# Optimization experiments

Measured on AMD Instinct MI355X. Metric: run time of the kernel, lower is better.

Reference implementation:

```python
import jax, jax.numpy as jnp
import numpy as np

B, S, E, H, W = 1, 4096, 1024, 16, 256
D = E // H
SCALE = D ** -0.5


def setup_inputs() -> dict:
    key = jax.random.key(0)
    k1, k2, k3 = jax.random.split(key, 3)
    x = jax.random.normal(k1, (B, S, E), dtype=jnp.float32)
    # torch Linear weight is [out,in]; we store transposed [in,out] so y = x @ w
    w_qkv = jax.random.normal(k2, (E, 3 * E), dtype=jnp.float32) * (E ** -0.5)
    w_out = jax.random.normal(k3, (E, E), dtype=jnp.float32) * (E ** -0.5)
    # sliding-window causal mask: key j allowed for query i iff i-W < j <= i
    q_idx = jnp.arange(S)[:, None]
    k_idx = jnp.arange(S)[None, :]
    allowed_mask = (k_idx <= q_idx) & (k_idx > q_idx - W)  # [S,S] bool
    allowed_mask = allowed_mask[None, None]  # [1,1,S,S]
    return {"x": x, "allowed_mask": allowed_mask, "w_qkv": w_qkv, "w_out": w_out}


def reference(x, allowed_mask, w_qkv, w_out):
    b, s, e = x.shape
    qkv = (x @ w_qkv).reshape(b, s, 3, H, D)
    q, k, v = jnp.moveaxis(qkv, 2, 0)  # each [b,s,H,D]
    q = q.transpose(0, 2, 1, 3)  # [b,H,s,D]
    k = k.transpose(0, 2, 1, 3)
    v = v.transpose(0, 2, 1, 3)
    scores = jnp.einsum('bhsd,bhtd->bhst', q, k) * SCALE  # [b,H,s,s]
    scores = jnp.where(allowed_mask, scores, -jnp.inf)
    attn = jax.nn.softmax(scores, axis=-1)
    out = jnp.einsum('bhst,bhtd->bhsd', attn, v)  # [b,H,s,D]
    out = out.transpose(0, 2, 1, 3).reshape(b, s, e)
    return out @ w_out
```

## Files before the change

kernel.cpp:

```cpp
#include <hip/hip_runtime.h>
#include <hip/hip_bf16.h>

#define S_LEN 4096
#define EMB   1024
#define NH    16
#define HD    64
#define WIN   256
#define SCALE 0.125f

typedef __attribute__((ext_vector_type(8))) short short8;
typedef __attribute__((ext_vector_type(4))) float f32x4;
typedef __attribute__((ext_vector_type(4))) unsigned short us4;

__device__ inline unsigned short f2b(float x) {
    __hip_bfloat16 b = __float2bfloat16(x);
    return *reinterpret_cast<unsigned short*>(&b);
}

__device__ inline void gld_lds16(const unsigned short* g, unsigned short* l) {
    __builtin_amdgcn_global_load_lds(
        (const __attribute__((address_space(1))) unsigned int*)g,
        (__attribute__((address_space(3))) unsigned int*)l,
        16, 0, 0);
}

__device__ inline void transpose_tile(const float* __restrict__ in,
                                      unsigned short* __restrict__ out,
                                      int R, int C, int bx, int by,
                                      unsigned short* t) {
    const int tid = threadIdx.x;
    const int r0 = by * 64, c0 = bx * 64;

    const int rr = tid >> 4, cc = (tid & 15) * 4;
    #pragma unroll
    for (int i = 0; i < 4; ++i) {
        float4 v = *reinterpret_cast<const float4*>(&in[(size_t)(r0 + rr + i * 16) * C + c0 + cc]);
        t[(cc + 0) * 72 + rr + i * 16] = f2b(v.x);
        t[(cc + 1) * 72 + rr + i * 16] = f2b(v.y);
        t[(cc + 2) * 72 + rr + i * 16] = f2b(v.z);
        t[(cc + 3) * 72 + rr + i * 16] = f2b(v.w);
    }
    __syncthreads();

    const int wr = tid >> 2, wk = (tid & 3) * 16;
    #pragma unroll
    for (int p = 0; p < 2; ++p)
        *reinterpret_cast<uint4*>(&out[(size_t)(c0 + wr) * R + r0 + wk + p * 8]) =
            *reinterpret_cast<const uint4*>(&t[wr * 72 + wk + p * 8]);
}

__global__ __launch_bounds__(256) void prep(const float* __restrict__ x,
                                            unsigned short* __restrict__ xb,
                                            const float* __restrict__ w_qkv,
                                            unsigned short* __restrict__ wqkvT,
                                            const float* __restrict__ w_out,
                                            unsigned short* __restrict__ woutT) {
    __shared__ alignas(16) unsigned short t[64 * 72];
    const int b = blockIdx.x;
    if (b < 768) {
        transpose_tile(w_qkv, wqkvT, EMB, 3 * EMB, b % 48, b / 48, t);
    } else if (b < 1024) {
        const int bb = b - 768;
        transpose_tile(w_out, woutT, EMB, EMB, bb & 15, bb >> 4, t);
    } else {
        const size_t tt = (size_t)(b - 1024) * 256 + threadIdx.x;
        const float4* s4 = reinterpret_cast<const float4*>(x) + tt * 4;
        float4 v0 = s4[0], v1 = s4[1], v2 = s4[2], v3 = s4[3];
        us4 p0 = {f2b(v0.x), f2b(v0.y), f2b(v0.z), f2b(v0.w)};
        us4 p1 = {f2b(v1.x), f2b(v1.y), f2b(v1.z), f2b(v1.w)};
        us4 p2 = {f2b(v2.x), f2b(v2.y), f2b(v2.z), f2b(v2.w)};
        us4 p3 = {f2b(v3.x), f2b(v3.y), f2b(v3.z), f2b(v3.w)};
        us4* d = reinterpret_cast<us4*>(xb) + tt * 4;
        d[0] = p0; d[1] = p1; d[2] = p2; d[3] = p3;
    }
}

template <int MODE, int BN>
__global__ __launch_bounds__(256) void gemm_bt(const unsigned short* __restrict__ A,
                                               const unsigned short* __restrict__ Bt,
                                               void* __restrict__ Cout,
                                               unsigned short* __restrict__ vT,
                                               int M, int N, int K) {
    constexpr int SMEM_ELEMS = (MODE == 1) ? 17408 : 8192 + BN * 64;
    constexpr int NJ = BN / 32;
    __shared__ alignas(16) unsigned short smem[SMEM_ELEMS];
    unsigned short* As = smem;
    unsigned short* Bs = smem + 8192;

    const int tid  = threadIdx.x;
    const int lane = tid & 63;
    const int w    = tid >> 6;
    const int quad = lane >> 4;
    const int l16  = lane & 15;

    const int m0 = blockIdx.y * 128;
    const int n0 = blockIdx.x * BN;
    const int m_off = (w & 1) * 64;
    const int n_off = (w >> 1) * (BN / 2);

    const int s_row = tid >> 3;
    const int s_c0  = tid & 7;

    f32x4 acc[4][NJ];
    #pragma unroll
    for (int i = 0; i < 4; ++i)
        #pragma unroll
        for (int j = 0; j < NJ; ++j)
            acc[i][j] = (f32x4){0.f, 0.f, 0.f, 0.f};

    for (int bk = 0; bk < K; bk += 64) {
        __syncthreads();
        #pragma unroll
        for (int p = 0; p < 4; ++p) {
            const int row = p * 32 + s_row;
            const int c   = s_c0 ^ (row & 7);
            gld_lds16(A + (size_t)(m0 + row) * K + bk + c * 8,
                      As + (p * 256 + w * 64) * 8);
        }
        #pragma unroll
        for (int p = 0; p < BN / 32; ++p) {
            const int row = p * 32 + s_row;
            const int c   = s_c0 ^ (row & 7);
            gld_lds16(Bt + (size_t)(n0 + row) * K + bk + c * 8,
                      Bs + (p * 256 + w * 64) * 8);
        }
        __syncthreads();

        #pragma unroll
        for (int ks = 0; ks < 2; ++ks) {
            short8 af[4], bf[NJ];
            #pragma unroll
            for (int i = 0; i < 4; ++i) {
                const int r = m_off + i * 16 + l16;
                af[i] = *reinterpret_cast<const short8*>(
                    &As[r * 64 + ((ks * 4 + quad) ^ (r & 7)) * 8]);
            }
            #pragma unroll
            for (int j = 0; j < NJ; ++j) {
                const int r = n_off + j * 16 + l16;
                bf[j] = *reinterpret_cast<const short8*>(
                    &Bs[r * 64 + ((ks * 4 + quad) ^ (r & 7)) * 8]);
            }
            #pragma unroll
            for (int i = 0; i < 4; ++i)
                #pragma unroll
                for (int j = 0; j < NJ; ++j)
                    acc[i][j] = __builtin_amdgcn_mfma_f32_16x16x32_bf16(
                        af[i], bf[j], acc[i][j], 0, 0, 0);
        }
    }

    if (MODE == 0) {
        float* C = (float*)Cout;
        #pragma unroll
        for (int i = 0; i < 4; ++i)
            #pragma unroll
            for (int r = 0; r < 4; ++r) {
                const size_t row = m0 + m_off + i * 16 + quad * 4 + r;
                #pragma unroll
                for (int j = 0; j < NJ; ++j)
                    C[row * N + n0 + n_off + j * 16 + l16] = acc[i][j][r];
            }
    } else if (n0 < 2048) {
        const float sc = (n0 < 1024) ? SCALE : 1.0f;
        unsigned short* C = (unsigned short*)Cout;
        #pragma unroll
        for (int i = 0; i < 4; ++i)
            #pragma unroll
            for (int r = 0; r < 4; ++r) {
                const size_t row = m0 + m_off + i * 16 + quad * 4 + r;
                #pragma unroll
                for (int j = 0; j < NJ; ++j)
                    C[row * N + n0 + n_off + j * 16 + l16] = f2b(acc[i][j][r] * sc);
            }
    } else {
        __syncthreads();
        #pragma unroll
        for (int i = 0; i < 4; ++i) {
            const int ss = m_off + i * 16 + quad * 4;
            #pragma unroll
            for (int j = 0; j < NJ; ++j) {
                const int dd = n_off + j * 16 + l16;
                us4 pk = {f2b(acc[i][j][0]), f2b(acc[i][j][1]),
                          f2b(acc[i][j][2]), f2b(acc[i][j][3])};
                *reinterpret_cast<us4*>(&smem[dd * 136 + ss]) = pk;
            }
        }
        __syncthreads();
        #pragma unroll
        for (int p = 0; p < 8; ++p) {
            const int t  = p * 256 + tid;
            const int dd = t >> 4;
            const int sc2 = (t & 15) * 8;
            *reinterpret_cast<uint4*>(&vT[(size_t)(n0 - 2048 + dd) * S_LEN + m0 + sc2]) =
                *reinterpret_cast<const uint4*>(&smem[dd * 136 + sc2]);
        }
    }
}

__global__ __launch_bounds__(256) void attn_mfma(const unsigned short* __restrict__ qkv,
                                                 const unsigned short* __restrict__ vT,
                                                 unsigned short* __restrict__ outb) {
    __shared__ alignas(16) unsigned short lds[40960];
    unsigned short* KtP = lds;
    unsigned short* Vt  = lds + 20480;

    const int raw  = blockIdx.x + (blockIdx.y << 6);
    const int xcd  = raw & 7;
    const int slot = raw >> 3;
    const int q0   = (xcd * 8 + (slot & 7)) * 64;
    const int h    = slot >> 3;

    const int tid  = threadIdx.x;
    const int w    = tid >> 6;
    const int lane = tid & 63;
    const int quad = lane >> 4;
    const int l16  = lane & 15;
    const int kbase = q0 - 256;

    const unsigned short* qrow = qkv + (size_t)(q0 + w * 16 + l16) * 3072 + h * 64;
    short8 aq[2];
    aq[0] = *reinterpret_cast<const short8*>(qrow + quad * 8);
    aq[1] = *reinterpret_cast<const short8*>(qrow + 32 + quad * 8);

    #pragma unroll
    for (int i = 0; i < 10; ++i) {
        const int fc  = i * 256 + tid;
        const int row = fc >> 3, p = fc & 7;
        const int c   = p ^ (row & 7);
        int j = kbase + row; if (j < 0) j = 0;
        gld_lds16(qkv + (size_t)j * 3072 + EMB + h * 64 + c * 8,
                  KtP + (i * 256 + w * 64) * 8);
    }

    __syncthreads();

    #pragma unroll
    for (int i = 0; i < 10; ++i) {
        const int fc = i * 256 + tid;
        const int d  = fc / 40, pp = fc % 40;
        const int cc = (pp & ~7) | ((pp & 7) ^ (d & 7));
        int j0 = kbase + cc * 8; if (j0 < 0) j0 = 0;
        gld_lds16(vT + (size_t)(h * 64 + d) * S_LEN + j0,
                  Vt + (i * 256 + w * 64) * 8);
    }

    f32x4 accs[17];
    #pragma unroll
    for (int nb = 0; nb < 17; ++nb) accs[nb] = (f32x4){0.f, 0.f, 0.f, 0.f};

    #pragma unroll
    for (int ks = 0; ks < 2; ++ks)
        #pragma unroll
        for (int nb = 0; nb < 17; ++nb) {
            const int row = (w + nb) * 16 + l16;
            const int p   = (ks * 4 + quad) ^ (l16 & 7);
            const short8 bfr = *reinterpret_cast<const short8*>(&KtP[row * 64 + p * 8]);
            accs[nb] = __builtin_amdgcn_mfma_f32_16x16x32_bf16(aq[ks], bfr, accs[nb], 0, 0, 0);
        }

    __syncthreads();

    const int i0 = q0 + w * 16 + quad * 4;
    const int rw0 = w * 16 + quad * 4;
    float rsum[4] = {0.f, 0.f, 0.f, 0.f};
    #pragma unroll
    for (int nb = 0; nb < 17; ++nb) {
        const int t   = w + nb;
        const int j   = kbase + t * 16 + l16;
        const int cch = (t * 16 + l16) >> 3, e = l16 & 7;
        #pragma unroll
        for (int r = 0; r < 4; ++r) {
            const int i = i0 + r;
            const bool ok = (j >= 0) & (j <= i) & (j > i - WIN);
            const float ev = ok ? __expf(accs[nb][r]) : 0.f;
            rsum[r] += ev;
            const int rw  = rw0 + r;
            const int pos = (cch & ~7) | ((cch & 7) ^ (rw & 7));
            KtP[rw * 320 + pos * 8 + e] = f2b(ev);
        }
    }
    {
        const int tz = (w & 1) ? (w - 1) : (w + 17);
        const int cch = (tz * 16 + l16) >> 3, e = l16 & 7;
        #pragma unroll
        for (int r = 0; r < 4; ++r) {
            const int rw  = rw0 + r;
            const int pos = (cch & ~7) | ((cch & 7) ^ (rw & 7));
            KtP[rw * 320 + pos * 8 + e] = 0;
        }
    }
    float inv[4];
    #pragma unroll
    for (int r = 0; r < 4; ++r) {
        float s = rsum[r];
        #pragma unroll
        for (int off = 1; off < 16; off <<= 1)
            s += __shfl_xor(s, off, 64);
        inv[r] = 1.f / s;
    }

    f32x4 acco[4];
    #pragma unroll
    for (int nb2 = 0; nb2 < 4; ++nb2) acco[nb2] = (f32x4){0.f, 0.f, 0.f, 0.f};

    const int ks0 = w >> 1;
    #pragma unroll
    for (int ksi = 0; ksi < 9; ++ksi) {
        const int ks   = ks0 + ksi;
        const int prow = w * 16 + l16;
        const int cc   = ks * 4 + quad;
        const int ppos = (cc & ~7) | ((cc & 7) ^ (prow & 7));
        const short8 af = *reinterpret_cast<const short8*>(&KtP[prow * 320 + ppos * 8]);
        #pragma unroll
        for (int nb2 = 0; nb2 < 4; ++nb2) {
            const int d    = nb2 * 16 + l16;
            const int vpos = (cc & ~7) | ((cc & 7) ^ (d & 7));
            const short8 bfr = *reinterpret_cast<const short8*>(&Vt[d * 320 + vpos * 8]);
            acco[nb2] = __builtin_amdgcn_mfma_f32_16x16x32_bf16(af, bfr, acco[nb2], 0, 0, 0);
        }
    }

    #pragma unroll
    for (int nb2 = 0; nb2 < 4; ++nb2)
        #pragma unroll
        for (int r = 0; r < 4; ++r)
            outb[(size_t)(q0 + w * 16 + quad * 4 + r) * EMB + h * 64 + nb2 * 16 + l16] =
                f2b(acco[nb2][r] * inv[r]);
}

extern "C" void kernel_launch(void* const* d_in, const int* in_sizes, int n_in,
                              void* d_out, int out_size, void* d_ws, size_t ws_size,
                              hipStream_t stream) {
    const float* x     = (const float*)d_in[0];
    const float* w_qkv = (const float*)d_in[2];
    const float* w_out = (const float*)d_in[3];
    float* out = (float*)d_out;

    char* ws = (char*)d_ws;
    unsigned short* xb     = (unsigned short*)(ws);
    unsigned short* wqkvT  = (unsigned short*)(ws + (8u  << 20));
    unsigned short* woutT  = (unsigned short*)(ws + (14u << 20));
    unsigned short* qkvb   = (unsigned short*)(ws + (16u << 20));
    unsigned short* attnb  = (unsigned short*)(ws + (48u << 20));
    unsigned short* vT     = (unsigned short*)(ws + (56u << 20));

    prep<<<2048, 256, 0, stream>>>(x, xb, w_qkv, wqkvT, w_out, woutT);

    gemm_bt<1, 128><<<dim3(3 * EMB / 128, S_LEN / 128), 256, 0, stream>>>(
        xb, wqkvT, qkvb, vT, S_LEN, 3 * EMB, EMB);

    attn_mfma<<<dim3(S_LEN / 64, NH), 256, 0, stream>>>(qkvb, vT, attnb);

    gemm_bt<0, 64><<<dim3(EMB / 64, S_LEN / 128), 256, 0, stream>>>(
        attnb, woutT, out, nullptr, S_LEN, EMB, EMB);
}
```

Before: 189.3 us.

## Replace QKV projection GEMM with 256x256-tile, 512-thread, 4-stage pipelined kernel

Adds a dedicated QKV GEMM kernel that uses 256x256 output tiles with 8 waves, a 4-stage global-to-LDS async pipeline with XOR-swizzled shared memory, and raised priority around the MFMA block. It also writes the V transpose through a swizzled LDS staging buffer. The aim is more data reuse per tile and better overlap of loads with matrix math than the generic 128-tile GEMM. The cost is that only 192 blocks are launched, fewer than the CU count, and 128 KB of LDS is used per block, which limits occupancy.

```diff
diff --git a/kernel.cpp b/kernel.cpp
--- a/kernel.cpp
+++ b/kernel.cpp
@@ -198,6 +198,137 @@
     }
 }
 
+__global__ __launch_bounds__(512) void gemm_qkv(const unsigned short* __restrict__ A,
+                                                const unsigned short* __restrict__ Bt,
+                                                unsigned short* __restrict__ C,
+                                                unsigned short* __restrict__ vT) {
+    __shared__ alignas(16) unsigned short smem[65536];
+
+    constexpr int K = EMB;
+    const int tid  = threadIdx.x;
+    const int lane = tid & 63;
+    const int w    = tid >> 6;
+    const int quad = lane >> 4;
+    const int l16  = lane & 15;
+    const int wr   = w >> 2, wc = w & 3;
+    const int wm0  = wr * 128, wn0 = wc * 64;
+
+    const int raw = blockIdx.x;
+    const int s   = (raw & 7) * 24 + (raw >> 3);
+    const int by  = s / 12, bx = s % 12;
+    const int m0  = by * 256, n0 = bx * 256;
+
+    const int srow = tid >> 2;
+    const int scp  = tid & 3;
+    const int sc4  = scp ^ ((srow >> 1) & 3);
+    const unsigned short* pA = A  + (size_t)(m0 + srow) * K + sc4 * 8;
+    const unsigned short* pB = Bt + (size_t)(n0 + srow) * K + sc4 * 8;
+    const int dls = (w * 64) * 8;
+
+    auto STAGE = [&](int q) {
+        unsigned short* dA = smem + ((q >> 1) & 1) * 32768 + (q & 1) * 8192 + dls;
+        unsigned short* dB = dA + 16384;
+        const int gk = q * 32;
+        gld_lds16(pA + gk, dA);
+        gld_lds16(pA + (size_t)128 * K + gk, dA + 4096);
+        gld_lds16(pB + gk, dB);
+        gld_lds16(pB + (size_t)128 * K + gk, dB + 4096);
+    };
+
+    const int cpf = quad ^ ((l16 >> 1) & 3);
+    const int oA  = (wm0 + l16) * 32 + cpf * 8;
+    const int oB  = (wn0 + l16) * 32 + cpf * 8;
+
+    f32x4 acc[8][4];
+    #pragma unroll
+    for (int i = 0; i < 8; ++i)
+        #pragma unroll
+        for (int j = 0; j < 4; ++j)
+            acc[i][j] = (f32x4){0.f, 0.f, 0.f, 0.f};
+
+    auto PHASE = [&](int p, bool stage_ok) {
+        const unsigned short* Ab = smem + ((p >> 1) & 1) * 32768 + (p & 1) * 8192;
+        const unsigned short* Bb = Ab + 16384;
+        short8 af[8], bf[4];
+        #pragma unroll
+        for (int i = 0; i < 8; ++i)
+            af[i] = *reinterpret_cast<const short8*>(&Ab[oA + i * 512]);
+        #pragma unroll
+        for (int j = 0; j < 4; ++j)
+            bf[j] = *reinterpret_cast<const short8*>(&Bb[oB + j * 512]);
+        if (stage_ok) STAGE(p + 3);
+        __builtin_amdgcn_sched_barrier(0);
+        __builtin_amdgcn_s_setprio(1);
+        #pragma unroll
+        for (int i = 0; i < 8; ++i)
+            #pragma unroll
+            for (int j = 0; j < 4; ++j)
+                acc[i][j] = __builtin_amdgcn_mfma_f32_16x16x32_bf16(af[i], bf[j], acc[i][j], 0, 0, 0);
+        __builtin_amdgcn_s_setprio(0);
+    };
+
+    STAGE(0); STAGE(1); STAGE(2);
+    asm volatile("s_waitcnt vmcnt(8)" ::: "memory");
+    __builtin_amdgcn_s_barrier();
+
+    for (int pp = 0; pp < 28; pp += 4) {
+        #pragma unroll
+        for (int e = 0; e < 4; ++e) {
+            PHASE(pp + e, true);
+            asm volatile("s_waitcnt vmcnt(8)" ::: "memory");
+            __builtin_amdgcn_s_barrier();
+        }
+    }
+    PHASE(28, true);
+    asm volatile("s_waitcnt vmcnt(8)" ::: "memory");
+    __builtin_amdgcn_s_barrier();
+    PHASE(29, false);
+    asm volatile("s_waitcnt vmcnt(4)" ::: "memory");
+    __builtin_amdgcn_s_barrier();
+    PHASE(30, false);
+    asm volatile("s_waitcnt vmcnt(0)" ::: "memory");
+    __builtin_amdgcn_s_barrier();
+    PHASE(31, false);
+    __builtin_amdgcn_s_barrier();
+
+    const int sec = n0 >> 10;
+    if (sec < 2) {
+        const float sc = (sec == 0) ? SCALE : 1.0f;
+        #pragma unroll
+        for (int i = 0; i < 8; ++i) {
+            #pragma unroll
+            for (int r = 0; r < 4; ++r) {
+                const size_t row = (size_t)(m0 + wm0 + i * 16 + quad * 4 + r) * 3072;
+                #pragma unroll
+                for (int j = 0; j < 4; ++j)
+                    C[row + n0 + wn0 + j * 16 + l16] = f2b(acc[i][j][r] * sc);
+            }
+        }
+    } else {
+        #pragma unroll
+        for (int i = 0; i < 8; ++i) {
+            const int ss = wm0 + i * 16 + quad * 4;
+            const int sc0 = ss >> 3, se = ss & 7;
+            #pragma unroll
+            for (int j = 0; j < 4; ++j) {
+                const int d = wn0 + j * 16 + l16;
+                us4 pk = {f2b(acc[i][j][0]), f2b(acc[i][j][1]),
+                          f2b(acc[i][j][2]), f2b(acc[i][j][3])};
+                *reinterpret_cast<us4*>(&smem[d * 256 + ((sc0 ^ (d & 31)) << 3) + se]) = pk;
+            }
+        }
+        __builtin_amdgcn_s_barrier();
+        const int vb = n0 - 2048;
+        #pragma unroll
+        for (int rep = 0; rep < 16; ++rep) {
+            const int idx = rep * 512 + tid;
+            const int d = idx >> 5, scr = idx & 31;
+            *reinterpret_cast<uint4*>(&vT[(size_t)(vb + d) * S_LEN + m0 + scr * 8]) =
+                *reinterpret_cast<const uint4*>(&smem[d * 256 + ((scr ^ (d & 31)) << 3)]);
+        }
+    }
+}
+
 __global__ __launch_bounds__(256) void attn_mfma(const unsigned short* __restrict__ qkv,
                                                  const unsigned short* __restrict__ vT,
                                                  unsigned short* __restrict__ outb) {
@@ -347,8 +478,7 @@
 
     prep<<<2048, 256, 0, stream>>>(x, xb, w_qkv, wqkvT, w_out, woutT);
 
-    gemm_bt<1, 128><<<dim3(3 * EMB / 128, S_LEN / 128), 256, 0, stream>>>(
-        xb, wqkvT, qkvb, vT, S_LEN, 3 * EMB, EMB);
+    gemm_qkv<<<dim3(192), 512, 0, stream>>>(xb, wqkvT, qkvb, vT);
 
     attn_mfma<<<dim3(S_LEN / 64, NH), 256, 0, stream>>>(qkvb, vT, attnb);
 
```

Result: faster. 184.4 us (-2.6%).
